# Optimization experiments

Hardware: AMD Instinct MI355X
Metric: run time of the kernel (lower is better)

Reference implementation:

```python
import jax, jax.numpy as jnp
import numpy as np

D_MODEL = 1024
NUM_HEADS = 16
D_K = D_MODEL // NUM_HEADS


def setup_inputs() -> dict:
    key = jax.random.key(0)
    ks = jax.random.split(key, 9)
    s = 1.0 / np.sqrt(D_MODEL)
    return {
        "z": jax.random.normal(ks[0], (4, 2048, D_MODEL), dtype=jnp.float32),
        "Wq": jax.random.uniform(ks[1], (D_MODEL, D_MODEL), jnp.float32, -s, s),
        "bq": jax.random.uniform(ks[2], (D_MODEL,), jnp.float32, -s, s),
        "Wk": jax.random.uniform(ks[3], (D_MODEL, D_MODEL), jnp.float32, -s, s),
        "bk": jax.random.uniform(ks[4], (D_MODEL,), jnp.float32, -s, s),
        "Wv": jax.random.uniform(ks[5], (D_MODEL, D_MODEL), jnp.float32, -s, s),
        "bv": jax.random.uniform(ks[6], (D_MODEL,), jnp.float32, -s, s),
        "Wo": jax.random.uniform(ks[7], (D_MODEL, D_MODEL), jnp.float32, -s, s),
        "bo": jax.random.uniform(ks[8], (D_MODEL,), jnp.float32, -s, s),
    }


def reference(z, Wq, bq, Wk, bk, Wv, bv, Wo, bo):
    B, S, _ = z.shape
    # project and split heads: [B, H, S, d_k]
    def proj(W, b):
        return (z @ W.T + b).reshape(B, S, NUM_HEADS, D_K).transpose(0, 2, 1, 3)
    Q, K, V = proj(Wq, bq), proj(Wk, bk), proj(Wv, bv)
    scale = 1.0 / np.sqrt(D_K)
    scores = jnp.einsum('bhqd,bhkd->bhqk', Q, K) * scale
    probs = jax.nn.softmax(scores, axis=-1)
    ctx = jnp.einsum('bhqk,bhkd->bhqd', probs, V)
    ctx = ctx.transpose(0, 2, 1, 3).reshape(B, S, D_MODEL)
    return ctx @ Wo.T + bo
```

## Files before the change

kernel.cpp:

```cpp
#include <hip/hip_runtime.h>
#include <stdint.h>

#define D_MODEL 1024
#define NHEAD 16
#define DKH 64
#define BATCH 4
#define SEQ 2048
#define M_ROWS (BATCH*SEQ)
#define NBH (BATCH*NHEAD)

typedef float f32x4 __attribute__((ext_vector_type(4)));
typedef float f32x16 __attribute__((ext_vector_type(16)));
typedef __bf16 bf16x8 __attribute__((ext_vector_type(8)));
typedef short short4v __attribute__((ext_vector_type(4)));
typedef unsigned short ushort4v __attribute__((ext_vector_type(4)));
typedef unsigned short ushort8v __attribute__((ext_vector_type(8)));
typedef int int2v __attribute__((ext_vector_type(2)));
typedef int int4v __attribute__((ext_vector_type(4)));

__device__ __forceinline__ unsigned short f2bf(float x) {
    __bf16 b = (__bf16)x;
    return __builtin_bit_cast(unsigned short, b);
}
__device__ __forceinline__ unsigned int packbf2(float lo, float hi) {
    return (unsigned int)f2bf(lo) | ((unsigned int)f2bf(hi) << 16);
}

#define GLL(gsrc, ldst) \
    __builtin_amdgcn_global_load_lds((const __attribute__((address_space(1))) void*)(gsrc), \
                                     (__attribute__((address_space(3))) void*)(ldst), 16, 0, 0)


__device__ __forceinline__ void cvt8store(const float* __restrict__ src,
                                          unsigned short* __restrict__ dst) {
    float4 v0 = *(const float4*)(src);
    float4 v1 = *(const float4*)(src + 4);
    ushort8v o;
    o[0] = f2bf(v0.x); o[1] = f2bf(v0.y); o[2] = f2bf(v0.z); o[3] = f2bf(v0.w);
    o[4] = f2bf(v1.x); o[5] = f2bf(v1.y); o[6] = f2bf(v1.z); o[7] = f2bf(v1.w);
    *(ushort8v*)dst = o;
}

__global__ __launch_bounds__(256) void k_convert(
    const float* __restrict__ z,  const float* __restrict__ wq,
    const float* __restrict__ wk, const float* __restrict__ wv,
    const float* __restrict__ wo,
    const float* __restrict__ bq, const float* __restrict__ bk,
    const float* __restrict__ bv,
    unsigned short* __restrict__ zf, unsigned short* __restrict__ wqkvf,
    unsigned short* __restrict__ wobf, float* __restrict__ biasf)
{
    int i = blockIdx.x * 256 + threadIdx.x;
    if (i < 1048576) {
        int lane = i & 63, rest = i >> 6;
        int kk = rest & 1, mfrag = (rest >> 1) & 7, half = (rest >> 4) & 1;
        int kt = (rest >> 5) & 15, mtile = rest >> 9;
        int row = mtile * 256 + half * 128 + mfrag * 16 + (lane & 15);
        int k = kt * 64 + kk * 32 + (lane >> 4) * 8;
        cvt8store(z + (size_t)row * 1024 + k, zf + (size_t)i * 8);
    }
    int i2 = i - 1048576;
    if (i2 >= 0 && i2 < 393216) {
        int lane = i2 & 63, rest = i2 >> 6;
        int kk = rest & 1, nfrag = (rest >> 1) & 7;
        int kt = (rest >> 4) & 15, ntile = rest >> 8;
        int n = ntile * 128 + nfrag * 16 + (lane & 15);
        int k = kt * 64 + kk * 32 + (lane >> 4) * 8;
        const float* W = (n < 1024) ? wq : ((n < 2048) ? wk : wv);
        cvt8store(W + (size_t)(n & 1023) * 1024 + k, wqkvf + (size_t)i2 * 8);
    }
    int i3 = i2 - 393216;
    if (i3 >= 0 && i3 < 131072) {
        int lane = i3 & 63, rest = i3 >> 6;
        int kk = rest & 1, nfrag = (rest >> 1) & 7;
        int kt = (rest >> 4) & 15, ntile = rest >> 8;
        int n = ntile * 128 + nfrag * 16 + (lane & 15);
        int k = kt * 64 + kk * 32 + (lane >> 4) * 8;
        cvt8store(wo + (size_t)n * 1024 + k, wobf + (size_t)i3 * 8);
    }
    if (i < 1024) {
        biasf[i]        = bq[i];
        biasf[1024 + i] = bk[i];
        biasf[2048 + i] = bv[i];
    }
}

__device__ __forceinline__ void g_stage(const unsigned short* __restrict__ as_,
                                        const unsigned short* __restrict__ bs_,
                                        unsigned short* la, unsigned short* lb,
                                        int wid, int lane)
{
#pragma unroll
    for (int g = 0; g < 4; ++g)
        GLL(as_ + (wid + 8 * g) * 512 + lane * 8, la + (wid + 8 * g) * 512);
#pragma unroll
    for (int g = 0; g < 2; ++g)
        GLL(bs_ + (wid + 8 * g) * 512 + lane * 8, lb + (wid + 8 * g) * 512);
}

#define GEMM_KLOOP(Abase, Bbase)                                                      \
    g_stage(Abase, Bbase, &ldsA[0][0], &ldsB[0][0], wid, lane);                       \
    g_stage(Abase + 16384, Bbase + 8192, &ldsA[1][0], &ldsB[1][0], wid, lane);        \
    asm volatile("s_waitcnt vmcnt(6)" ::: "memory");                                  \
    __builtin_amdgcn_s_barrier();                                                     \
    for (int t = 0; t < 16; ++t) {                                                    \
        int buf = t % 3;                                                              \
        if (t + 2 < 16)                                                               \
            g_stage(Abase + (size_t)(t + 2) * 16384, Bbase + (size_t)(t + 2) * 8192,  \
                    &ldsA[(t + 2) % 3][0], &ldsB[(t + 2) % 3][0], wid, lane);         \
        const unsigned short* A = &ldsA[buf][0];                                      \
        const unsigned short* B = &ldsB[buf][0];                                      \
        bf16x8 b00 = *(const bf16x8*)(B + ((wn * 2 + 0) * 2 + 0) * 512 + lane * 8);   \
        bf16x8 b01 = *(const bf16x8*)(B + ((wn * 2 + 0) * 2 + 1) * 512 + lane * 8);   \
        bf16x8 b10 = *(const bf16x8*)(B + ((wn * 2 + 1) * 2 + 0) * 512 + lane * 8);   \
        bf16x8 b11 = *(const bf16x8*)(B + ((wn * 2 + 1) * 2 + 1) * 512 + lane * 8);   \
        _Pragma("unroll")                                                             \
        for (int ii = 0; ii < 8; ++ii) {                                              \
            bf16x8 a0 = *(const bf16x8*)(A + ((wm * 8 + ii) * 2 + 0) * 512 + lane * 8); \
            bf16x8 a1 = *(const bf16x8*)(A + ((wm * 8 + ii) * 2 + 1) * 512 + lane * 8); \
            acc[ii][0] = __builtin_amdgcn_mfma_f32_16x16x32_bf16(a0, b00, acc[ii][0], 0, 0, 0); \
            acc[ii][0] = __builtin_amdgcn_mfma_f32_16x16x32_bf16(a1, b01, acc[ii][0], 0, 0, 0); \
            acc[ii][1] = __builtin_amdgcn_mfma_f32_16x16x32_bf16(a0, b10, acc[ii][1], 0, 0, 0); \
            acc[ii][1] = __builtin_amdgcn_mfma_f32_16x16x32_bf16(a1, b11, acc[ii][1], 0, 0, 0); \
        }                                                                             \
        if (t < 14)       { asm volatile("s_waitcnt vmcnt(6)" ::: "memory"); }        \
        else if (t == 14) { asm volatile("s_waitcnt vmcnt(0)" ::: "memory"); }        \
        if (t < 15) { __builtin_amdgcn_sched_barrier(0); __builtin_amdgcn_s_barrier(); } \
    }

__global__ __launch_bounds__(512) void k_gemm_qkv(
    const unsigned short* __restrict__ Af,
    const unsigned short* __restrict__ Bf,
    const float* __restrict__ biasf,
    unsigned short* __restrict__ qb, unsigned short* __restrict__ kfrag,
    unsigned short* __restrict__ vfrag)
{
    __shared__ unsigned short ldsA[3][16384];
    __shared__ unsigned short ldsB[3][8192];

    int bid = blockIdx.x;
    int wg = (bid & 7) * 96 + (bid >> 3);
    int tn = wg % 24, tm = wg / 24;
    int tid = threadIdx.x, wid = tid >> 6, lane = tid & 63;
    int wm = wid >> 2, wn = wid & 3;

    const unsigned short* Abase = Af + (size_t)tm * 16 * 16384;
    const unsigned short* Bbase = Bf + (size_t)tn * 16 * 8192;

    f32x4 acc[8][2] = {};
    GEMM_KLOOP(Abase, Bbase)

    const float QSC = 0.18033688011112042f;
    int t3 = tn >> 3;
#pragma unroll
    for (int j = 0; j < 2; ++j) {
        int col = tn * 128 + wn * 32 + j * 16 + (lane & 15);
        float bias = biasf[col];
        int d = col & 1023, h = d >> 6, dk = d & 63;
#pragma unroll
        for (int i = 0; i < 8; ++i) {
#pragma unroll
            for (int r = 0; r < 4; ++r) {
                int row = tm * 256 + wm * 128 + i * 16 + (lane >> 4) * 4 + r;
                float v = acc[i][j][r] + bias;
                if (t3 == 0) v *= QSC;
                unsigned short bv16 = f2bf(v);
                int b_ = row >> 11, s_ = row & 2047;
                int bh = b_ * NHEAD + h;
                if (t3 == 0) {
                    qb[((size_t)bh * SEQ + s_) * DKH + dk] = bv16;
                } else if (t3 == 1) {
                    int kvblk = s_ >> 6, r64 = s_ & 63;
                    int t32 = r64 >> 5, l5 = r64 & 31;
                    int ds = dk >> 4, hi2 = (dk >> 3) & 1, e = dk & 7;
                    kfrag[((size_t)(bh * 32 + kvblk)) * 4096 +
                          (t32 * 4 + ds) * 512 + (hi2 * 32 + l5) * 8 + e] = bv16;
                } else {
                    int kvblk = s_ >> 6, kv64 = s_ & 63;
                    int s16 = kv64 >> 4, hi2 = (kv64 >> 3) & 1, e = kv64 & 7;
                    int vt = dk >> 5, l5 = dk & 31;
                    vfrag[((size_t)(bh * 32 + kvblk)) * 4096 +
                          (vt * 4 + s16) * 512 + (hi2 * 32 + l5) * 8 + e] = bv16;
                }
            }
        }
    }
}

#define ATTN_STEP(LDSK, LDSV, WPREV, WCUR, DO_PV)                                   \
    {                                                                               \
        f32x16 st0 = {}, st1 = {};                                                  \
        __builtin_amdgcn_s_setprio(1);                                              \
        _Pragma("unroll")                                                           \
        for (int ds = 0; ds < 4; ++ds) {                                            \
            bf16x8 kf0 = *(const bf16x8*)(&(LDSK)[(ds) * 512 + lane * 8]);          \
            bf16x8 kf1 = *(const bf16x8*)(&(LDSK)[(4 + ds) * 512 + lane * 8]);      \
            st0 = __builtin_amdgcn_mfma_f32_32x32x16_bf16(kf0, aq[ds], st0, 0, 0, 0); \
            st1 = __builtin_amdgcn_mfma_f32_32x32x16_bf16(kf1, aq[ds], st1, 0, 0, 0); \
            if (DO_PV) {                                                            \
                bf16x8 vf0 = *(const bf16x8*)(&(LDSV)[(ds) * 512 + lane * 8]);      \
                bf16x8 vf1 = *(const bf16x8*)(&(LDSV)[(4 + ds) * 512 + lane * 8]);  \
                oa0 = __builtin_amdgcn_mfma_f32_32x32x16_bf16(vf0, WPREV[ds], oa0, 0, 0, 0); \
                oa1 = __builtin_amdgcn_mfma_f32_32x32x16_bf16(vf1, WPREV[ds], oa1, 0, 0, 0); \
            }                                                                       \
        }                                                                           \
        __builtin_amdgcn_s_setprio(0);                                              \
        unsigned int w16[16];                                                       \
        _Pragma("unroll")                                                           \
        for (int jj = 0; jj < 8; ++jj) {                                            \
            float p0 = __builtin_amdgcn_exp2f(st0[2 * jj]);                         \
            float p1 = __builtin_amdgcn_exp2f(st0[2 * jj + 1]);                     \
            lsum += p0 + p1;                                                        \
            w16[jj] = packbf2(p0, p1);                                              \
        }                                                                           \
        _Pragma("unroll")                                                           \
        for (int jj = 0; jj < 8; ++jj) {                                            \
            float p0 = __builtin_amdgcn_exp2f(st1[2 * jj]);                         \
            float p1 = __builtin_amdgcn_exp2f(st1[2 * jj + 1]);                     \
            lsum += p0 + p1;                                                        \
            w16[8 + jj] = packbf2(p0, p1);                                          \
        }                                                                           \
        _Pragma("unroll")                                                           \
        for (int s = 0; s < 4; ++s) {                                               \
            int base = (s >> 1) * 8 + (s & 1) * 4;                                  \
            int2v r1 = __builtin_amdgcn_permlane32_swap((int)w16[base + 0], (int)w16[base + 2], false, false); \
            int2v r2 = __builtin_amdgcn_permlane32_swap((int)w16[base + 1], (int)w16[base + 3], false, false); \
            int4v fr; fr[0] = r1[0]; fr[1] = r2[0]; fr[2] = r1[1]; fr[3] = r2[1];   \
            WCUR[s] = __builtin_bit_cast(bf16x8, fr);                               \
        }                                                                           \
    }

#define DRAIN_BARRIER()                                         \
    asm volatile("s_waitcnt vmcnt(0)" ::: "memory");            \
    __builtin_amdgcn_sched_barrier(0);                          \
    __builtin_amdgcn_s_barrier();

__global__ __launch_bounds__(512) void k_attn(
    const unsigned short* __restrict__ qg,
    const unsigned short* __restrict__ kb,
    const unsigned short* __restrict__ vtb,
    unsigned short* __restrict__ ctxf)
{
    __shared__ unsigned short lds_k[2][4096];
    __shared__ unsigned short lds_v[2][4096];

    int bid = blockIdx.x;
    int x = bid & 7, li = bid >> 3;
    int bh = x * 8 + (li >> 3);
    int qt = li & 7;

    int tid = threadIdx.x, wid = tid >> 6, lane = tid & 63;
    int lq = lane & 31, hi = lane >> 5;

    bf16x8 aq[4];
    {
        const unsigned short* qp = qg + ((size_t)bh * SEQ + qt * 256 + wid * 32 + lq) * DKH + hi * 8;
#pragma unroll
        for (int d = 0; d < 4; ++d) aq[d] = *(const bf16x8*)(qp + d * 16);
    }

    float lsum = 0.f;
    f32x16 oa0 = {};
    f32x16 oa1 = {};
    bf16x8 wA[4], wB[4];

    const unsigned short* kbase = kb  + (size_t)bh * 32 * 4096;
    const unsigned short* vbase = vtb + (size_t)bh * 32 * 4096;
    int so = wid * 512 + lane * 8;
    unsigned short* ldk0 = &lds_k[0][wid * 512];
    unsigned short* ldk1 = &lds_k[1][wid * 512];
    unsigned short* ldv0 = &lds_v[0][wid * 512];
    unsigned short* ldv1 = &lds_v[1][wid * 512];

    GLL(kbase + so, ldk0);
    DRAIN_BARRIER();

    GLL(kbase + 4096 + so, ldk1);
    GLL(vbase + so, ldv0);
    ATTN_STEP(lds_k[0], lds_v[0], wB, wA, false);
    DRAIN_BARRIER();

    for (int t = 1; t < 31; t += 2) {
        GLL(kbase + (size_t)(t + 1) * 4096 + so, ldk0);
        GLL(vbase + (size_t)t * 4096 + so, ldv1);
        ATTN_STEP(lds_k[1], lds_v[0], wA, wB, true);
        DRAIN_BARRIER();
        if (t + 2 < 32) GLL(kbase + (size_t)(t + 2) * 4096 + so, ldk1);
        GLL(vbase + (size_t)(t + 1) * 4096 + so, ldv0);
        ATTN_STEP(lds_k[0], lds_v[1], wB, wA, true);
        DRAIN_BARRIER();
    }

    GLL(vbase + (size_t)31 * 4096 + so, ldv1);
    ATTN_STEP(lds_k[1], lds_v[0], wA, wB, true);
    DRAIN_BARRIER();

    __builtin_amdgcn_s_setprio(1);
#pragma unroll
    for (int s = 0; s < 4; ++s) {
        bf16x8 vf0 = *(const bf16x8*)(&lds_v[1][(s) * 512 + lane * 8]);
        bf16x8 vf1 = *(const bf16x8*)(&lds_v[1][(4 + s) * 512 + lane * 8]);
        oa0 = __builtin_amdgcn_mfma_f32_32x32x16_bf16(vf0, wB[s], oa0, 0, 0, 0);
        oa1 = __builtin_amdgcn_mfma_f32_32x32x16_bf16(vf1, wB[s], oa1, 0, 0, 0);
    }
    __builtin_amdgcn_s_setprio(0);

    int b_ = bh >> 4, h = bh & 15;
    lsum += __shfl_xor(lsum, 32);
    float inv = 1.0f / lsum;
    int s_ = qt * 256 + wid * 32 + lq;
    int row = b_ * 2048 + s_;
    int mtile = row >> 8, half = (row >> 7) & 1, mfrag = (row >> 4) & 7, lrow = row & 15;
    unsigned short* cb = ctxf + (size_t)((mtile * 16 + h) * 2 + half) * 8192
                              + mfrag * 1024 + lrow * 8 + 4 * hi;
#pragma unroll
    for (int m = 0; m < 4; ++m) {
        ushort4v s0, s1;
        s0[0] = f2bf(oa0[4 * m + 0] * inv); s0[1] = f2bf(oa0[4 * m + 1] * inv);
        s0[2] = f2bf(oa0[4 * m + 2] * inv); s0[3] = f2bf(oa0[4 * m + 3] * inv);
        *(ushort4v*)(cb + m * 128) = s0;
        s1[0] = f2bf(oa1[4 * m + 0] * inv); s1[1] = f2bf(oa1[4 * m + 1] * inv);
        s1[2] = f2bf(oa1[4 * m + 2] * inv); s1[3] = f2bf(oa1[4 * m + 3] * inv);
        *(ushort4v*)(cb + 512 + m * 128) = s1;
    }
}

__global__ __launch_bounds__(512) void k_gemm_out(
    const unsigned short* __restrict__ Af,
    const unsigned short* __restrict__ Bf,
    const float* __restrict__ bo,
    float* __restrict__ out)
{
    __shared__ unsigned short ldsA[3][16384];
    __shared__ unsigned short ldsB[3][8192];

    int bid = blockIdx.x;
    int wg = (bid & 7) * 32 + (bid >> 3);
    int tn = wg % 8, tm = wg / 8;
    int tid = threadIdx.x, wid = tid >> 6, lane = tid & 63;
    int wm = wid >> 2, wn = wid & 3;

    const unsigned short* Abase = Af + (size_t)tm * 16 * 16384;
    const unsigned short* Bbase = Bf + (size_t)tn * 16 * 8192;

    f32x4 acc[8][2] = {};
    GEMM_KLOOP(Abase, Bbase)

#pragma unroll
    for (int j = 0; j < 2; ++j) {
        int col = tn * 128 + wn * 32 + j * 16 + (lane & 15);
        float bias = bo[col];
#pragma unroll
        for (int i = 0; i < 8; ++i) {
#pragma unroll
            for (int r = 0; r < 4; ++r) {
                int row = tm * 256 + wm * 128 + i * 16 + (lane >> 4) * 4 + r;
                out[(size_t)row * 1024 + col] = acc[i][j][r] + bias;
            }
        }
    }
}

extern "C" void kernel_launch(void* const* d_in, const int* in_sizes, int n_in,
                              void* d_out, int out_size, void* d_ws, size_t ws_size,
                              hipStream_t stream)
{
    const float* z  = (const float*)d_in[0];
    const float* Wq = (const float*)d_in[1];
    const float* bq = (const float*)d_in[2];
    const float* Wk = (const float*)d_in[3];
    const float* bk = (const float*)d_in[4];
    const float* Wv = (const float*)d_in[5];
    const float* bv = (const float*)d_in[6];
    const float* Wo = (const float*)d_in[7];
    const float* bo = (const float*)d_in[8];
    float* out = (float*)d_out;

    char* ws = (char*)d_ws;
    unsigned short* zf    = (unsigned short*)(ws);
    unsigned short* ctxf  = (unsigned short*)(ws);
    unsigned short* wqkvf = (unsigned short*)(ws + (16ull << 20));
    unsigned short* wobf  = (unsigned short*)(ws + (22ull << 20));
    float*          biasf = (float*)(ws + (24ull << 20));
    unsigned short* qb    = (unsigned short*)(ws + (25ull << 20));
    unsigned short* kfrag = (unsigned short*)(ws + (41ull << 20));
    unsigned short* vfrag = (unsigned short*)(ws + (57ull << 20));

    k_convert<<<8192, 256, 0, stream>>>(z, Wq, Wk, Wv, Wo, bq, bk, bv, zf, wqkvf, wobf, biasf);
    k_gemm_qkv<<<768, 512, 0, stream>>>(zf, wqkvf, biasf, qb, kfrag, vfrag);
    k_attn<<<NBH * 8, 512, 0, stream>>>(qb, kfrag, vfrag, ctxf);
    k_gemm_out<<<256, 512, 0, stream>>>(ctxf, wobf, bo, out);
}
```

Baseline: 214.6 us.

## Halve GEMM K-step to 32 and shrink LDS buffers for higher occupancy

Changes the pre-packed fragment layout of z, the weights and ctx from 64-wide to 32-wide K tiles, so each pipeline stage loads half as much data and the triple-buffered LDS footprint is halved. Both GEMM kernels now run 32 K-iterations with one MFMA pair per row-fragment, and launch bounds request 4 blocks per CU to gain occupancy. The trade-off is twice as many barriers and waitcnt stalls per tile, with less MFMA work between them to hide load latency.

New measurement: 226.3 us. 5.5% more time.

```diff
diff --git a/kernel.cpp b/kernel.cpp
--- a/kernel.cpp
+++ b/kernel.cpp
@@ -53,29 +53,29 @@
     int i = blockIdx.x * 256 + threadIdx.x;
     if (i < 1048576) {
         int lane = i & 63, rest = i >> 6;
-        int kk = rest & 1, mfrag = (rest >> 1) & 7, half = (rest >> 4) & 1;
-        int kt = (rest >> 5) & 15, mtile = rest >> 9;
+        int mfrag = rest & 7, half = (rest >> 3) & 1;
+        int kt = (rest >> 4) & 31, mtile = rest >> 9;
         int row = mtile * 256 + half * 128 + mfrag * 16 + (lane & 15);
-        int k = kt * 64 + kk * 32 + (lane >> 4) * 8;
+        int k = kt * 32 + (lane >> 4) * 8;
         cvt8store(z + (size_t)row * 1024 + k, zf + (size_t)i * 8);
     }
     int i2 = i - 1048576;
     if (i2 >= 0 && i2 < 393216) {
         int lane = i2 & 63, rest = i2 >> 6;
-        int kk = rest & 1, nfrag = (rest >> 1) & 7;
-        int kt = (rest >> 4) & 15, ntile = rest >> 8;
+        int nfrag = rest & 7;
+        int kt = (rest >> 3) & 31, ntile = rest >> 8;
         int n = ntile * 128 + nfrag * 16 + (lane & 15);
-        int k = kt * 64 + kk * 32 + (lane >> 4) * 8;
+        int k = kt * 32 + (lane >> 4) * 8;
         const float* W = (n < 1024) ? wq : ((n < 2048) ? wk : wv);
         cvt8store(W + (size_t)(n & 1023) * 1024 + k, wqkvf + (size_t)i2 * 8);
     }
     int i3 = i2 - 393216;
     if (i3 >= 0 && i3 < 131072) {
         int lane = i3 & 63, rest = i3 >> 6;
-        int kk = rest & 1, nfrag = (rest >> 1) & 7;
-        int kt = (rest >> 4) & 15, ntile = rest >> 8;
+        int nfrag = rest & 7;
+        int kt = (rest >> 3) & 31, ntile = rest >> 8;
         int n = ntile * 128 + nfrag * 16 + (lane & 15);
-        int k = kt * 64 + kk * 32 + (lane >> 4) * 8;
+        int k = kt * 32 + (lane >> 4) * 8;
         cvt8store(wo + (size_t)n * 1024 + k, wobf + (size_t)i3 * 8);
     }
     if (i < 1024) {
@@ -85,58 +85,50 @@
     }
 }
 
-__device__ __forceinline__ void g_stage(const unsigned short* __restrict__ as_,
-                                        const unsigned short* __restrict__ bs_,
-                                        unsigned short* la, unsigned short* lb,
-                                        int wid, int lane)
-{
-#pragma unroll
-    for (int g = 0; g < 4; ++g)
-        GLL(as_ + (wid + 8 * g) * 512 + lane * 8, la + (wid + 8 * g) * 512);
-#pragma unroll
-    for (int g = 0; g < 2; ++g)
-        GLL(bs_ + (wid + 8 * g) * 512 + lane * 8, lb + (wid + 8 * g) * 512);
-}
-
-#define GEMM_KLOOP(Abase, Bbase)                                                      \
-    g_stage(Abase, Bbase, &ldsA[0][0], &ldsB[0][0], wid, lane);                       \
-    g_stage(Abase + 16384, Bbase + 8192, &ldsA[1][0], &ldsB[1][0], wid, lane);        \
-    asm volatile("s_waitcnt vmcnt(6)" ::: "memory");                                  \
+__device__ __forceinline__ void g_stage32(const unsigned short* __restrict__ as_,
+                                          const unsigned short* __restrict__ bs_,
+                                          unsigned short* la, unsigned short* lb,
+                                          int wid, int lane)
+{
+    GLL(as_ + (wid * 2 + 0) * 512 + lane * 8, la + (wid * 2 + 0) * 512);
+    GLL(as_ + (wid * 2 + 1) * 512 + lane * 8, la + (wid * 2 + 1) * 512);
+    GLL(bs_ + wid * 512 + lane * 8, lb + wid * 512);
+}
+
+#define GEMM_KLOOP32(Abase, Bbase)                                                    \
+    g_stage32(Abase, Bbase, &ldsA[0][0], &ldsB[0][0], wid, lane);                     \
+    g_stage32(Abase + 8192, Bbase + 4096, &ldsA[1][0], &ldsB[1][0], wid, lane);       \
+    asm volatile("s_waitcnt vmcnt(3)" ::: "memory");                                  \
     __builtin_amdgcn_s_barrier();                                                     \
-    for (int t = 0; t < 16; ++t) {                                                    \
+    for (int t = 0; t < 32; ++t) {                                                    \
         int buf = t % 3;                                                              \
-        if (t + 2 < 16)                                                               \
-            g_stage(Abase + (size_t)(t + 2) * 16384, Bbase + (size_t)(t + 2) * 8192,  \
-                    &ldsA[(t + 2) % 3][0], &ldsB[(t + 2) % 3][0], wid, lane);         \
+        if (t + 2 < 32)                                                               \
+            g_stage32(Abase + (size_t)(t + 2) * 8192, Bbase + (size_t)(t + 2) * 4096, \
+                      &ldsA[(t + 2) % 3][0], &ldsB[(t + 2) % 3][0], wid, lane);       \
         const unsigned short* A = &ldsA[buf][0];                                      \
         const unsigned short* B = &ldsB[buf][0];                                      \
-        bf16x8 b00 = *(const bf16x8*)(B + ((wn * 2 + 0) * 2 + 0) * 512 + lane * 8);   \
-        bf16x8 b01 = *(const bf16x8*)(B + ((wn * 2 + 0) * 2 + 1) * 512 + lane * 8);   \
-        bf16x8 b10 = *(const bf16x8*)(B + ((wn * 2 + 1) * 2 + 0) * 512 + lane * 8);   \
-        bf16x8 b11 = *(const bf16x8*)(B + ((wn * 2 + 1) * 2 + 1) * 512 + lane * 8);   \
+        bf16x8 b0 = *(const bf16x8*)(B + (wn * 2 + 0) * 512 + lane * 8);              \
+        bf16x8 b1 = *(const bf16x8*)(B + (wn * 2 + 1) * 512 + lane * 8);              \
         _Pragma("unroll")                                                             \
         for (int ii = 0; ii < 8; ++ii) {                                              \
-            bf16x8 a0 = *(const bf16x8*)(A + ((wm * 8 + ii) * 2 + 0) * 512 + lane * 8); \
-            bf16x8 a1 = *(const bf16x8*)(A + ((wm * 8 + ii) * 2 + 1) * 512 + lane * 8); \
-            acc[ii][0] = __builtin_amdgcn_mfma_f32_16x16x32_bf16(a0, b00, acc[ii][0], 0, 0, 0); \
-            acc[ii][0] = __builtin_amdgcn_mfma_f32_16x16x32_bf16(a1, b01, acc[ii][0], 0, 0, 0); \
-            acc[ii][1] = __builtin_amdgcn_mfma_f32_16x16x32_bf16(a0, b10, acc[ii][1], 0, 0, 0); \
-            acc[ii][1] = __builtin_amdgcn_mfma_f32_16x16x32_bf16(a1, b11, acc[ii][1], 0, 0, 0); \
+            bf16x8 a = *(const bf16x8*)(A + (wm * 8 + ii) * 512 + lane * 8);          \
+            acc[ii][0] = __builtin_amdgcn_mfma_f32_16x16x32_bf16(a, b0, acc[ii][0], 0, 0, 0); \
+            acc[ii][1] = __builtin_amdgcn_mfma_f32_16x16x32_bf16(a, b1, acc[ii][1], 0, 0, 0); \
         }                                                                             \
-        if (t < 14)       { asm volatile("s_waitcnt vmcnt(6)" ::: "memory"); }        \
-        else if (t == 14) { asm volatile("s_waitcnt vmcnt(0)" ::: "memory"); }        \
-        if (t < 15) { __builtin_amdgcn_sched_barrier(0); __builtin_amdgcn_s_barrier(); } \
-    }
-
-__global__ __launch_bounds__(512) void k_gemm_qkv(
+        if (t < 30)       { asm volatile("s_waitcnt vmcnt(3)" ::: "memory"); }        \
+        else if (t == 30) { asm volatile("s_waitcnt vmcnt(0)" ::: "memory"); }        \
+        if (t < 31) { __builtin_amdgcn_sched_barrier(0); __builtin_amdgcn_s_barrier(); } \
+    }
+
+__global__ __launch_bounds__(512, 4) void k_gemm_qkv(
     const unsigned short* __restrict__ Af,
     const unsigned short* __restrict__ Bf,
     const float* __restrict__ biasf,
     unsigned short* __restrict__ qb, unsigned short* __restrict__ kfrag,
     unsigned short* __restrict__ vfrag)
 {
-    __shared__ unsigned short ldsA[3][16384];
-    __shared__ unsigned short ldsB[3][8192];
+    __shared__ unsigned short ldsA[3][8192];
+    __shared__ unsigned short ldsB[3][4096];
 
     int bid = blockIdx.x;
     int wg = (bid & 7) * 96 + (bid >> 3);
@@ -144,17 +136,17 @@
     int tid = threadIdx.x, wid = tid >> 6, lane = tid & 63;
     int wm = wid >> 2, wn = wid & 3;
 
-    const unsigned short* Abase = Af + (size_t)tm * 16 * 16384;
-    const unsigned short* Bbase = Bf + (size_t)tn * 16 * 8192;
+    const unsigned short* Abase = Af + (size_t)tm * 32 * 8192;
+    const unsigned short* Bbase = Bf + (size_t)tn * 32 * 4096;
 
     f32x4 acc[8][2] = {};
-    GEMM_KLOOP(Abase, Bbase)
+    GEMM_KLOOP32(Abase, Bbase)
 
     const float QSC = 0.18033688011112042f;
     int t3 = tn >> 3;
 #pragma unroll
     for (int j = 0; j < 2; ++j) {
-        int col = tn * 128 + wn * 32 + j * 16 + (lane & 15);
+        int col = tn * 128 + (wn * 2 + j) * 16 + (lane & 15);
         float bias = biasf[col];
         int d = col & 1023, h = d >> 6, dk = d & 63;
 #pragma unroll
@@ -311,8 +303,8 @@
     int s_ = qt * 256 + wid * 32 + lq;
     int row = b_ * 2048 + s_;
     int mtile = row >> 8, half = (row >> 7) & 1, mfrag = (row >> 4) & 7, lrow = row & 15;
-    unsigned short* cb = ctxf + (size_t)((mtile * 16 + h) * 2 + half) * 8192
-                              + mfrag * 1024 + lrow * 8 + 4 * hi;
+    unsigned short* cb = ctxf + ((size_t)((mtile * 32 + h * 2) * 16 + half * 8 + mfrag)) * 512
+                              + lrow * 8 + 4 * hi;
 #pragma unroll
     for (int m = 0; m < 4; ++m) {
         ushort4v s0, s1;
@@ -321,18 +313,18 @@
         *(ushort4v*)(cb + m * 128) = s0;
         s1[0] = f2bf(oa1[4 * m + 0] * inv); s1[1] = f2bf(oa1[4 * m + 1] * inv);
         s1[2] = f2bf(oa1[4 * m + 2] * inv); s1[3] = f2bf(oa1[4 * m + 3] * inv);
-        *(ushort4v*)(cb + 512 + m * 128) = s1;
-    }
-}
-
-__global__ __launch_bounds__(512) void k_gemm_out(
+        *(ushort4v*)(cb + 8192 + m * 128) = s1;
+    }
+}
+
+__global__ __launch_bounds__(512, 4) void k_gemm_out(
     const unsigned short* __restrict__ Af,
     const unsigned short* __restrict__ Bf,
     const float* __restrict__ bo,
     float* __restrict__ out)
 {
-    __shared__ unsigned short ldsA[3][16384];
-    __shared__ unsigned short ldsB[3][8192];
+    __shared__ unsigned short ldsA[3][8192];
+    __shared__ unsigned short ldsB[3][4096];
 
     int bid = blockIdx.x;
     int wg = (bid & 7) * 32 + (bid >> 3);
@@ -340,15 +332,15 @@
     int tid = threadIdx.x, wid = tid >> 6, lane = tid & 63;
     int wm = wid >> 2, wn = wid & 3;
 
-    const unsigned short* Abase = Af + (size_t)tm * 16 * 16384;
-    const unsigned short* Bbase = Bf + (size_t)tn * 16 * 8192;
+    const unsigned short* Abase = Af + (size_t)tm * 32 * 8192;
+    const unsigned short* Bbase = Bf + (size_t)tn * 32 * 4096;
 
     f32x4 acc[8][2] = {};
-    GEMM_KLOOP(Abase, Bbase)
+    GEMM_KLOOP32(Abase, Bbase)
 
 #pragma unroll
     for (int j = 0; j < 2; ++j) {
-        int col = tn * 128 + wn * 32 + j * 16 + (lane & 15);
+        int col = tn * 128 + (wn * 2 + j) * 16 + (lane & 15);
         float bias = bo[col];
 #pragma unroll
         for (int i = 0; i < 8; ++i) {
```

## Load K/V fragments directly from global memory instead of LDS double-buffering

Applied to the files above, without the earlier changes.

Replaces the LDS double-buffered K/V pipeline, with its per-step barriers and software-pipelined PV overlap, with per-wave direct global loads of pre-fragmented K and V tiles into registers. All 8 waves of a block read the same K/V tiles and rely on L1/L2 to serve the duplicate reads. This removes LDS traffic and block-wide barriers. In exchange it loses the cross-step overlap of QK and PV and exposes global load latency inside each iteration, and it multiplies cache traffic.

Result: faster. 209.6 us (-2.3%).

```diff
diff --git a/kernel.cpp b/kernel.cpp
--- a/kernel.cpp
+++ b/kernel.cpp
@@ -187,63 +187,12 @@
     }
 }
 
-#define ATTN_STEP(LDSK, LDSV, WPREV, WCUR, DO_PV)                                   \
-    {                                                                               \
-        f32x16 st0 = {}, st1 = {};                                                  \
-        __builtin_amdgcn_s_setprio(1);                                              \
-        _Pragma("unroll")                                                           \
-        for (int ds = 0; ds < 4; ++ds) {                                            \
-            bf16x8 kf0 = *(const bf16x8*)(&(LDSK)[(ds) * 512 + lane * 8]);          \
-            bf16x8 kf1 = *(const bf16x8*)(&(LDSK)[(4 + ds) * 512 + lane * 8]);      \
-            st0 = __builtin_amdgcn_mfma_f32_32x32x16_bf16(kf0, aq[ds], st0, 0, 0, 0); \
-            st1 = __builtin_amdgcn_mfma_f32_32x32x16_bf16(kf1, aq[ds], st1, 0, 0, 0); \
-            if (DO_PV) {                                                            \
-                bf16x8 vf0 = *(const bf16x8*)(&(LDSV)[(ds) * 512 + lane * 8]);      \
-                bf16x8 vf1 = *(const bf16x8*)(&(LDSV)[(4 + ds) * 512 + lane * 8]);  \
-                oa0 = __builtin_amdgcn_mfma_f32_32x32x16_bf16(vf0, WPREV[ds], oa0, 0, 0, 0); \
-                oa1 = __builtin_amdgcn_mfma_f32_32x32x16_bf16(vf1, WPREV[ds], oa1, 0, 0, 0); \
-            }                                                                       \
-        }                                                                           \
-        __builtin_amdgcn_s_setprio(0);                                              \
-        unsigned int w16[16];                                                       \
-        _Pragma("unroll")                                                           \
-        for (int jj = 0; jj < 8; ++jj) {                                            \
-            float p0 = __builtin_amdgcn_exp2f(st0[2 * jj]);                         \
-            float p1 = __builtin_amdgcn_exp2f(st0[2 * jj + 1]);                     \
-            lsum += p0 + p1;                                                        \
-            w16[jj] = packbf2(p0, p1);                                              \
-        }                                                                           \
-        _Pragma("unroll")                                                           \
-        for (int jj = 0; jj < 8; ++jj) {                                            \
-            float p0 = __builtin_amdgcn_exp2f(st1[2 * jj]);                         \
-            float p1 = __builtin_amdgcn_exp2f(st1[2 * jj + 1]);                     \
-            lsum += p0 + p1;                                                        \
-            w16[8 + jj] = packbf2(p0, p1);                                          \
-        }                                                                           \
-        _Pragma("unroll")                                                           \
-        for (int s = 0; s < 4; ++s) {                                               \
-            int base = (s >> 1) * 8 + (s & 1) * 4;                                  \
-            int2v r1 = __builtin_amdgcn_permlane32_swap((int)w16[base + 0], (int)w16[base + 2], false, false); \
-            int2v r2 = __builtin_amdgcn_permlane32_swap((int)w16[base + 1], (int)w16[base + 3], false, false); \
-            int4v fr; fr[0] = r1[0]; fr[1] = r2[0]; fr[2] = r1[1]; fr[3] = r2[1];   \
-            WCUR[s] = __builtin_bit_cast(bf16x8, fr);                               \
-        }                                                                           \
-    }
-
-#define DRAIN_BARRIER()                                         \
-    asm volatile("s_waitcnt vmcnt(0)" ::: "memory");            \
-    __builtin_amdgcn_sched_barrier(0);                          \
-    __builtin_amdgcn_s_barrier();
-
 __global__ __launch_bounds__(512) void k_attn(
     const unsigned short* __restrict__ qg,
     const unsigned short* __restrict__ kb,
     const unsigned short* __restrict__ vtb,
     unsigned short* __restrict__ ctxf)
 {
-    __shared__ unsigned short lds_k[2][4096];
-    __shared__ unsigned short lds_v[2][4096];
-
     int bid = blockIdx.x;
     int x = bid & 7, li = bid >> 3;
     int bh = x * 8 + (li >> 3);
@@ -262,48 +211,63 @@
     float lsum = 0.f;
     f32x16 oa0 = {};
     f32x16 oa1 = {};
-    bf16x8 wA[4], wB[4];
-
-    const unsigned short* kbase = kb  + (size_t)bh * 32 * 4096;
-    const unsigned short* vbase = vtb + (size_t)bh * 32 * 4096;
-    int so = wid * 512 + lane * 8;
-    unsigned short* ldk0 = &lds_k[0][wid * 512];
-    unsigned short* ldk1 = &lds_k[1][wid * 512];
-    unsigned short* ldv0 = &lds_v[0][wid * 512];
-    unsigned short* ldv1 = &lds_v[1][wid * 512];
-
-    GLL(kbase + so, ldk0);
-    DRAIN_BARRIER();
-
-    GLL(kbase + 4096 + so, ldk1);
-    GLL(vbase + so, ldv0);
-    ATTN_STEP(lds_k[0], lds_v[0], wB, wA, false);
-    DRAIN_BARRIER();
-
-    for (int t = 1; t < 31; t += 2) {
-        GLL(kbase + (size_t)(t + 1) * 4096 + so, ldk0);
-        GLL(vbase + (size_t)t * 4096 + so, ldv1);
-        ATTN_STEP(lds_k[1], lds_v[0], wA, wB, true);
-        DRAIN_BARRIER();
-        if (t + 2 < 32) GLL(kbase + (size_t)(t + 2) * 4096 + so, ldk1);
-        GLL(vbase + (size_t)(t + 1) * 4096 + so, ldv0);
-        ATTN_STEP(lds_k[0], lds_v[1], wB, wA, true);
-        DRAIN_BARRIER();
-    }
-
-    GLL(vbase + (size_t)31 * 4096 + so, ldv1);
-    ATTN_STEP(lds_k[1], lds_v[0], wA, wB, true);
-    DRAIN_BARRIER();
-
-    __builtin_amdgcn_s_setprio(1);
-#pragma unroll
-    for (int s = 0; s < 4; ++s) {
-        bf16x8 vf0 = *(const bf16x8*)(&lds_v[1][(s) * 512 + lane * 8]);
-        bf16x8 vf1 = *(const bf16x8*)(&lds_v[1][(4 + s) * 512 + lane * 8]);
-        oa0 = __builtin_amdgcn_mfma_f32_32x32x16_bf16(vf0, wB[s], oa0, 0, 0, 0);
-        oa1 = __builtin_amdgcn_mfma_f32_32x32x16_bf16(vf1, wB[s], oa1, 0, 0, 0);
-    }
-    __builtin_amdgcn_s_setprio(0);
+
+    const unsigned short* kp = kb  + (size_t)bh * 32 * 4096 + lane * 8;
+    const unsigned short* vp = vtb + (size_t)bh * 32 * 4096 + lane * 8;
+
+    for (int kt = 0; kt < 32; ++kt) {
+        bf16x8 kf[8];
+#pragma unroll
+        for (int f = 0; f < 8; ++f) kf[f] = *(const bf16x8*)(kp + f * 512);
+
+        f32x16 st0 = {}, st1 = {};
+        __builtin_amdgcn_s_setprio(1);
+#pragma unroll
+        for (int ds = 0; ds < 4; ++ds) {
+            st0 = __builtin_amdgcn_mfma_f32_32x32x16_bf16(kf[ds],     aq[ds], st0, 0, 0, 0);
+            st1 = __builtin_amdgcn_mfma_f32_32x32x16_bf16(kf[4 + ds], aq[ds], st1, 0, 0, 0);
+        }
+        __builtin_amdgcn_s_setprio(0);
+
+        bf16x8 vf[8];
+#pragma unroll
+        for (int f = 0; f < 8; ++f) vf[f] = *(const bf16x8*)(vp + f * 512);
+
+        unsigned int w16[16];
+#pragma unroll
+        for (int jj = 0; jj < 8; ++jj) {
+            float p0 = __builtin_amdgcn_exp2f(st0[2 * jj]);
+            float p1 = __builtin_amdgcn_exp2f(st0[2 * jj + 1]);
+            lsum += p0 + p1;
+            w16[jj] = packbf2(p0, p1);
+        }
+#pragma unroll
+        for (int jj = 0; jj < 8; ++jj) {
+            float p0 = __builtin_amdgcn_exp2f(st1[2 * jj]);
+            float p1 = __builtin_amdgcn_exp2f(st1[2 * jj + 1]);
+            lsum += p0 + p1;
+            w16[8 + jj] = packbf2(p0, p1);
+        }
+        bf16x8 w[4];
+#pragma unroll
+        for (int s = 0; s < 4; ++s) {
+            int base = (s >> 1) * 8 + (s & 1) * 4;
+            int2v r1 = __builtin_amdgcn_permlane32_swap((int)w16[base + 0], (int)w16[base + 2], false, false);
+            int2v r2 = __builtin_amdgcn_permlane32_swap((int)w16[base + 1], (int)w16[base + 3], false, false);
+            int4v fr; fr[0] = r1[0]; fr[1] = r2[0]; fr[2] = r1[1]; fr[3] = r2[1];
+            w[s] = __builtin_bit_cast(bf16x8, fr);
+        }
+
+        __builtin_amdgcn_s_setprio(1);
+#pragma unroll
+        for (int s = 0; s < 4; ++s) {
+            oa0 = __builtin_amdgcn_mfma_f32_32x32x16_bf16(vf[s],     w[s], oa0, 0, 0, 0);
+            oa1 = __builtin_amdgcn_mfma_f32_32x32x16_bf16(vf[4 + s], w[s], oa1, 0, 0, 0);
+        }
+        __builtin_amdgcn_s_setprio(0);
+
+        kp += 4096; vp += 4096;
+    }
 
     int b_ = bh >> 4, h = bh & 15;
     lsum += __shfl_xor(lsum, 32);
```
